# Kernel optimization log

Measured on AMD Instinct MI355X. Metric: run time of the kernel, lower is better.

Reference implementation:

```python
import jax, jax.numpy as jnp
import numpy as np
from jax.scipy.linalg import expm

DELTA = 0.01  # time step from __init__ delta
B_SZ, U_DIM, DU_DIM, H_DIM, Y_DIM = 512, 1024, 512, 2048, 1024


def setup_inputs() -> dict:
    key = jax.random.key(0)
    ks = jax.random.split(key, 6)
    inv_sqrt = lambda fan_in: 1.0 / np.sqrt(fan_in)
    u = jax.random.normal(ks[0], (B_SZ, U_DIM), jnp.float32)
    du = jax.random.normal(ks[1], (B_SZ, DU_DIM), jnp.float32)
    # torch.nn.Linear default init: U(-1/sqrt(fan_in), 1/sqrt(fan_in))
    W = jax.random.uniform(ks[2], (H_DIM, H_DIM), jnp.float32, -inv_sqrt(H_DIM), inv_sqrt(H_DIM))
    Bw = jax.random.uniform(ks[3], (H_DIM, U_DIM + DU_DIM), jnp.float32, -inv_sqrt(U_DIM + DU_DIM), inv_sqrt(U_DIM + DU_DIM))
    Cw = jax.random.uniform(ks[4], (Y_DIM, H_DIM), jnp.float32, -inv_sqrt(H_DIM), inv_sqrt(H_DIM))
    h = jax.random.normal(ks[5], (1, H_DIM), jnp.float32)
    return {"u": u, "du": du, "W": W, "Bw": Bw, "Cw": Cw, "h": h}


def reference(u, du, W, Bw, Cw, h):
    # Antisymmetric part of W
    A = 0.5 * (W - W.T)                                    # (H,H)
    A_expm = expm(A * DELTA)                               # (H,H) matrix exponential
    rec = h @ A_expm.T                                     # (1,H) recurrent term: F.linear(h, A_expm)
    A_inv = jnp.linalg.inv(A)                              # (H,H)
    # B(cat([du, u])) : (B, H)
    b = jnp.concatenate([du, u], axis=1) @ Bw.T
    # M = A^{-1} (expm(A*delta) - I); input term = M @ b^T per sample -> b @ M^T
    M = A_inv @ (A_expm - jnp.eye(H_DIM, dtype=A.dtype))   # (H,H)
    inp = b @ M.T                                          # (B,H)
    h_new = rec + inp                                      # broadcast (1,H)+(B,H) -> (B,H)
    y = h_new @ Cw.T                                       # (B,Y)
    return y
```

## Files before the change

### kernel.cpp

```cpp
#include <hip/hip_runtime.h>
#include <hip/hip_bf16.h>


#define B_SZ 512
#define U_DIM 1024
#define DU_DIM 512
#define H_DIM 2048
#define Y_DIM 1024
#define K_CAT 1536
#define DELTA_F 0.01f

typedef __hip_bfloat16 bf16;
using bf16x8f = __attribute__((ext_vector_type(8))) short;
using f32x4   = __attribute__((ext_vector_type(4))) float;

__device__ __forceinline__ short f2bs(float x) {
  union { bf16 b; short s; } u; u.b = __float2bfloat16(x); return u.s;
}
__device__ __forceinline__ int4 pack8(const float4 v0, const float4 v1) {
  union { short s[8]; int4 i; } o;
  o.s[0] = f2bs(v0.x); o.s[1] = f2bs(v0.y); o.s[2] = f2bs(v0.z); o.s[3] = f2bs(v0.w);
  o.s[4] = f2bs(v1.x); o.s[5] = f2bs(v1.y); o.s[6] = f2bs(v1.z); o.s[7] = f2bs(v1.w);
  return o.i;
}

#define LDP 72
#define LDS_SHORTS (2 * 32 * LDP + 2 * 64 * LDP)

template <int KDIM, int EPI>
__device__ __forceinline__ void gemm_tile(short* lds, const short* __restrict__ A,
                                          const short* __restrict__ B, const float* __restrict__ bias,
                                          float scale, void* __restrict__ out, int Ncols,
                                          int mt, int nt) {
  short* As0 = lds;
  short* Bs0 = lds + 2 * 32 * LDP;
  const int tid = threadIdx.x;
  const int lane = tid & 63, wave = tid >> 6;
  const int wm = wave >> 1, wn = wave & 1;
  const int row0 = mt * 32, col0 = nt * 64;
  const int rA = tid >> 3, kc = (tid & 7) * 8;
  f32x4 acc[2] = {};
  int4 pa, pb1, pb2;
  auto ldA  = [&](int kt) { return *(const int4*)(A + (size_t)(row0 + rA) * KDIM + kt * 64 + kc); };
  auto ldB1 = [&](int kt) { return *(const int4*)(B + (size_t)(col0 + rA) * KDIM + kt * 64 + kc); };
  auto ldB2 = [&](int kt) { return *(const int4*)(B + (size_t)(col0 + rA + 32) * KDIM + kt * 64 + kc); };
  pa = ldA(0); pb1 = ldB1(0); pb2 = ldB2(0);
  *(int4*)&As0[rA * LDP + kc] = pa;
  *(int4*)&Bs0[rA * LDP + kc] = pb1;
  *(int4*)&Bs0[(rA + 32) * LDP + kc] = pb2;
  const int NT = KDIM / 64;
  const int kq = (lane >> 4) * 8, rm = lane & 15;
  for (int kt = 0; kt < NT; kt++) {
    const int cur = kt & 1;
    if (kt + 1 < NT) { pa = ldA(kt + 1); pb1 = ldB1(kt + 1); pb2 = ldB2(kt + 1); }
    __syncthreads();
    const short* Ac = As0 + cur * (32 * LDP);
    const short* Bc = Bs0 + cur * (64 * LDP);
    bf16x8f af[2], bfr[2][2];
#pragma unroll
    for (int ks = 0; ks < 2; ks++) {
      af[ks] = *(const bf16x8f*)&Ac[(wm * 16 + rm) * LDP + ks * 32 + kq];
#pragma unroll
      for (int j = 0; j < 2; j++)
        bfr[ks][j] = *(const bf16x8f*)&Bc[(wn * 32 + 16 * j + rm) * LDP + ks * 32 + kq];
    }
#pragma unroll
    for (int ks = 0; ks < 2; ks++)
#pragma unroll
      for (int j = 0; j < 2; j++)
        acc[j] = __builtin_amdgcn_mfma_f32_16x16x32_bf16(af[ks], bfr[ks][j], acc[j], 0, 0, 0);
    if (kt + 1 < NT) {
      short* An = As0 + (cur ^ 1) * (32 * LDP);
      short* Bn = Bs0 + (cur ^ 1) * (64 * LDP);
      *(int4*)&An[rA * LDP + kc] = pa;
      *(int4*)&Bn[rA * LDP + kc] = pb1;
      *(int4*)&Bn[(rA + 32) * LDP + kc] = pb2;
      __syncthreads();
    }
  }
  const int quad = lane >> 4;
#pragma unroll
  for (int j = 0; j < 2; j++) {
    int gc = col0 + wn * 32 + 16 * j + rm;
#pragma unroll
    for (int r = 0; r < 4; r++) {
      int gr = row0 + wm * 16 + quad * 4 + r;
      float v = acc[j][r];
      if (EPI == 0) ((short*)out)[(size_t)gr * Ncols + gc] = f2bs(v);
      else          ((float*)out)[(size_t)gr * Ncols + gc] = bias[gc] + scale * v;
    }
  }
}

#define NZ (B_SZ * K_CAT / 8)
#define NB (H_DIM * K_CAT / 8)
#define NC (Y_DIM * H_DIM / 8)

__global__ __launch_bounds__(256) void k1(const float* __restrict__ W, const float* __restrict__ h,
                                          const float* __restrict__ du, const float* __restrict__ u,
                                          const float* __restrict__ Bw, const float* __restrict__ Cw,
                                          float* __restrict__ wh, float* __restrict__ wth,
                                          short* __restrict__ z, short* __restrict__ Bwb,
                                          short* __restrict__ Cwb) {
  const int b = blockIdx.x;
  if (b < 512) {
    const int lane = threadIdx.x & 63, wave = threadIdx.x >> 6;
    const int row = b * 4 + wave;
    const float* wr = W + (size_t)row * H_DIM;
    float s = 0.f;
#pragma unroll
    for (int it = 0; it < 8; it++) {
      int k = it * 256 + lane * 4;
      float4 a = *(const float4*)(wr + k);
      float4 hv = *(const float4*)(h + k);
      s += a.x * hv.x + a.y * hv.y + a.z * hv.z + a.w * hv.w;
    }
#pragma unroll
    for (int off = 32; off > 0; off >>= 1) s += __shfl_down(s, off);
    if (lane == 0) wh[row] = s;
  } else if (b < 768) {
    const int e = b - 512;
    const int colg = e & 7, rowg = e >> 3;
    const int k = colg * 256 + threadIdx.x;
    float s = 0.f;
    const float* base = W + (size_t)rowg * 64 * H_DIM + k;
#pragma unroll 8
    for (int i = 0; i < 64; i++) s += base[(size_t)i * H_DIM] * h[rowg * 64 + i];
    atomicAdd(&wth[k], s);
  } else {
    const int NG = NZ + NB + NC;
    for (int g = (b - 768) * 256 + threadIdx.x; g < NG; g += 512 * 256) {
      const float* src; short* dst;
      if (g < NZ) {
        int e = g * 8, row = e / K_CAT, col = e % K_CAT;
        src = (col < DU_DIM) ? du + (size_t)row * DU_DIM + col
                             : u + (size_t)row * U_DIM + (col - DU_DIM);
        dst = z + e;
      } else if (g < NZ + NB) {
        int e = (g - NZ) * 8; src = Bw + e; dst = Bwb + e;
      } else {
        int e = (g - NZ - NB) * 8; src = Cw + e; dst = Cwb + e;
      }
      *(int4*)dst = pack8(*(const float4*)src, *(const float4*)(src + 4));
    }
  }
}

__global__ __launch_bounds__(256) void k2(const short* __restrict__ z, const short* __restrict__ Bwb,
                                          short* __restrict__ bb, const float* __restrict__ Cw,
                                          const float* __restrict__ h, const float* __restrict__ wh,
                                          const float* __restrict__ wth, float* __restrict__ yrec) {
  __shared__ __align__(16) short lds[LDS_SHORTS];
  const int b = blockIdx.x;
  if (b < 512) {
    gemm_tile<K_CAT, 0>(lds, z, Bwb, nullptr, 0.f, bb, H_DIM, b >> 5, b & 31);
  } else {
    const int lane = threadIdx.x & 63, wave = threadIdx.x >> 6;
    const int row = (b - 512) * 4 + wave;
    const float* cr = Cw + (size_t)row * H_DIM;
    float s = 0.f;
#pragma unroll
    for (int it = 0; it < 8; it++) {
      int k = it * 256 + lane * 4;
      float4 c = *(const float4*)(cr + k);
      float4 hv = *(const float4*)(h + k);
      float4 a = *(const float4*)(wh + k);
      float4 bq = *(const float4*)(wth + k);
      s += c.x * (hv.x + 0.005f * (a.x - bq.x));
      s += c.y * (hv.y + 0.005f * (a.y - bq.y));
      s += c.z * (hv.z + 0.005f * (a.z - bq.z));
      s += c.w * (hv.w + 0.005f * (a.w - bq.w));
    }
#pragma unroll
    for (int off = 32; off > 0; off >>= 1) s += __shfl_down(s, off);
    if (lane == 0) yrec[row] = s;
  }
}

__global__ __launch_bounds__(256) void k3(const short* __restrict__ bb, const short* __restrict__ Cwb,
                                          const float* __restrict__ yrec, float* __restrict__ y) {
  __shared__ __align__(16) short lds[LDS_SHORTS];
  gemm_tile<H_DIM, 1>(lds, bb, Cwb, yrec, DELTA_F, y, Y_DIM, blockIdx.x >> 4, blockIdx.x & 15);
}

extern "C" void kernel_launch(void* const* d_in, const int* in_sizes, int n_in,
                              void* d_out, int out_size, void* d_ws, size_t ws_size,
                              hipStream_t stream) {
  const float* u  = (const float*)d_in[0];
  const float* du = (const float*)d_in[1];
  const float* W  = (const float*)d_in[2];
  const float* Bw = (const float*)d_in[3];
  const float* Cw = (const float*)d_in[4];
  const float* h  = (const float*)d_in[5];
  float* y = (float*)d_out;

  char* w = (char*)d_ws;
  size_t off = 0;
  short* z   = (short*)(w + off); off += (size_t)B_SZ * K_CAT * sizeof(short);
  short* Bwb = (short*)(w + off); off += (size_t)H_DIM * K_CAT * sizeof(short);
  short* Cwb = (short*)(w + off); off += (size_t)Y_DIM * H_DIM * sizeof(short);
  short* bb  = (short*)(w + off); off += (size_t)B_SZ * H_DIM * sizeof(short);
  float* wh  = (float*)(w + off); off += H_DIM * sizeof(float);
  float* wth = (float*)(w + off); off += H_DIM * sizeof(float);
  float* yrec= (float*)(w + off); off += Y_DIM * sizeof(float);
  if (ws_size < off) return;

  hipMemsetAsync(wth, 0, H_DIM * sizeof(float), stream);
  k1<<<1280, 256, 0, stream>>>(W, h, du, u, Bw, Cw, wh, wth, z, Bwb, Cwb);
  k2<<<768, 256, 0, stream>>>(z, Bwb, bb, Cw, h, wh, wth, yrec);
  k3<<<256, 256, 0, stream>>>(bb, Cwb, yrec, y);
}
```

Measured before the change: 123.4 us.

## Fold recurrent term into hidden state and replace atomics with partial sums

```diff
diff --git a/kernel.cpp b/kernel.cpp
--- a/kernel.cpp
+++ b/kernel.cpp
@@ -29,9 +29,11 @@
 
 template <int KDIM, int EPI>
 __device__ __forceinline__ void gemm_tile(short* lds, const short* __restrict__ A,
-                                          const short* __restrict__ B, const float* __restrict__ bias,
-                                          float scale, void* __restrict__ out, int Ncols,
-                                          int mt, int nt) {
+                                          const short* __restrict__ B,
+                                          const float* __restrict__ h, const float* __restrict__ wh,
+                                          const float* __restrict__ wtp,
+                                          void* __restrict__ out, int Ncols, int mt, int nt) {
+  __shared__ float recf[64];
   short* As0 = lds;
   short* Bs0 = lds + 2 * 32 * LDP;
   const int tid = threadIdx.x;
@@ -78,6 +80,16 @@
       __syncthreads();
     }
   }
+  if (EPI == 0) {
+    if (tid < 64) {
+      int gc = col0 + tid;
+      float s = 0.f;
+#pragma unroll
+      for (int p = 0; p < 32; p++) s += wtp[p * H_DIM + gc];
+      recf[tid] = h[gc] + 0.005f * (wh[gc] - s);
+    }
+    __syncthreads();
+  }
   const int quad = lane >> 4;
 #pragma unroll
   for (int j = 0; j < 2; j++) {
@@ -86,8 +98,8 @@
     for (int r = 0; r < 4; r++) {
       int gr = row0 + wm * 16 + quad * 4 + r;
       float v = acc[j][r];
-      if (EPI == 0) ((short*)out)[(size_t)gr * Ncols + gc] = f2bs(v);
-      else          ((float*)out)[(size_t)gr * Ncols + gc] = bias[gc] + scale * v;
+      if (EPI == 0) ((short*)out)[(size_t)gr * Ncols + gc] = f2bs(recf[gc - col0] + DELTA_F * v);
+      else          ((float*)out)[(size_t)gr * Ncols + gc] = v;
     }
   }
 }
@@ -99,7 +111,7 @@
 __global__ __launch_bounds__(256) void k1(const float* __restrict__ W, const float* __restrict__ h,
                                           const float* __restrict__ du, const float* __restrict__ u,
                                           const float* __restrict__ Bw, const float* __restrict__ Cw,
-                                          float* __restrict__ wh, float* __restrict__ wth,
+                                          float* __restrict__ wh, float* __restrict__ wtp,
                                           short* __restrict__ z, short* __restrict__ Bwb,
                                           short* __restrict__ Cwb) {
   const int b = blockIdx.x;
@@ -126,7 +138,7 @@
     const float* base = W + (size_t)rowg * 64 * H_DIM + k;
 #pragma unroll 8
     for (int i = 0; i < 64; i++) s += base[(size_t)i * H_DIM] * h[rowg * 64 + i];
-    atomicAdd(&wth[k], s);
+    wtp[rowg * H_DIM + k] = s;
   } else {
     const int NG = NZ + NB + NC;
     for (int g = (b - 768) * 256 + threadIdx.x; g < NG; g += 512 * 256) {
@@ -147,40 +159,16 @@
 }
 
 __global__ __launch_bounds__(256) void k2(const short* __restrict__ z, const short* __restrict__ Bwb,
-                                          short* __restrict__ bb, const float* __restrict__ Cw,
                                           const float* __restrict__ h, const float* __restrict__ wh,
-                                          const float* __restrict__ wth, float* __restrict__ yrec) {
+                                          const float* __restrict__ wtp, short* __restrict__ bb) {
   __shared__ __align__(16) short lds[LDS_SHORTS];
-  const int b = blockIdx.x;
-  if (b < 512) {
-    gemm_tile<K_CAT, 0>(lds, z, Bwb, nullptr, 0.f, bb, H_DIM, b >> 5, b & 31);
-  } else {
-    const int lane = threadIdx.x & 63, wave = threadIdx.x >> 6;
-    const int row = (b - 512) * 4 + wave;
-    const float* cr = Cw + (size_t)row * H_DIM;
-    float s = 0.f;
-#pragma unroll
-    for (int it = 0; it < 8; it++) {
-      int k = it * 256 + lane * 4;
-      float4 c = *(const float4*)(cr + k);
-      float4 hv = *(const float4*)(h + k);
-      float4 a = *(const float4*)(wh + k);
-      float4 bq = *(const float4*)(wth + k);
-      s += c.x * (hv.x + 0.005f * (a.x - bq.x));
-      s += c.y * (hv.y + 0.005f * (a.y - bq.y));
-      s += c.z * (hv.z + 0.005f * (a.z - bq.z));
-      s += c.w * (hv.w + 0.005f * (a.w - bq.w));
-    }
-#pragma unroll
-    for (int off = 32; off > 0; off >>= 1) s += __shfl_down(s, off);
-    if (lane == 0) yrec[row] = s;
-  }
+  gemm_tile<K_CAT, 0>(lds, z, Bwb, h, wh, wtp, bb, H_DIM, blockIdx.x >> 5, blockIdx.x & 31);
 }
 
 __global__ __launch_bounds__(256) void k3(const short* __restrict__ bb, const short* __restrict__ Cwb,
-                                          const float* __restrict__ yrec, float* __restrict__ y) {
+                                          float* __restrict__ y) {
   __shared__ __align__(16) short lds[LDS_SHORTS];
-  gemm_tile<H_DIM, 1>(lds, bb, Cwb, yrec, DELTA_F, y, Y_DIM, blockIdx.x >> 4, blockIdx.x & 15);
+  gemm_tile<H_DIM, 1>(lds, bb, Cwb, nullptr, nullptr, nullptr, y, Y_DIM, blockIdx.x >> 4, blockIdx.x & 15);
 }
 
 extern "C" void kernel_launch(void* const* d_in, const int* in_sizes, int n_in,
@@ -201,12 +189,10 @@
   short* Cwb = (short*)(w + off); off += (size_t)Y_DIM * H_DIM * sizeof(short);
   short* bb  = (short*)(w + off); off += (size_t)B_SZ * H_DIM * sizeof(short);
   float* wh  = (float*)(w + off); off += H_DIM * sizeof(float);
-  float* wth = (float*)(w + off); off += H_DIM * sizeof(float);
-  float* yrec= (float*)(w + off); off += Y_DIM * sizeof(float);
+  float* wtp = (float*)(w + off); off += 32 * H_DIM * sizeof(float);
   if (ws_size < off) return;
 
-  hipMemsetAsync(wth, 0, H_DIM * sizeof(float), stream);
-  k1<<<1280, 256, 0, stream>>>(W, h, du, u, Bw, Cw, wh, wth, z, Bwb, Cwb);
-  k2<<<768, 256, 0, stream>>>(z, Bwb, bb, Cw, h, wh, wth, yrec);
-  k3<<<256, 256, 0, stream>>>(bb, Cwb, yrec, y);
+  k1<<<1280, 256, 0, stream>>>(W, h, du, u, Bw, Cw, wh, wtp, z, Bwb, Cwb);
+  k2<<<512, 256, 0, stream>>>(z, Bwb, h, wh, wtp, bb);
+  k3<<<256, 256, 0, stream>>>(bb, Cwb, y);
 }
```

After: 123.1 us. Within noise of the previous version (-0.3%).
